# Kernel optimization log

Hardware: AMD Instinct MI355X
Metric: run time of the kernel (lower is better)

Reference implementation:

```python
import jax, jax.numpy as jnp
import numpy as np

LEFT = 16  # attention window size (previous `left` symbols incl. current)


def _make_history(symbols, left):
    """contexts[b, t, j] = symbols[b, t - (left-1-j)] for j in [0,left),
    padded with symbols[b, 0] for out-of-range positions (pad = symbols[:, :1])."""
    B, T = symbols.shape
    # (T, left) gather index matrix
    idx = jnp.arange(T)[:, None] - (left - 1 - jnp.arange(left))[None, :]
    valid = idx >= 0
    idx_c = jnp.clip(idx, 0, T - 1)
    ctx = symbols[:, idx_c]                                   # (B, T, left)
    pad = symbols[:, :1][:, :, None]                          # (B, 1, 1)
    return jnp.where(valid[None, :, :], ctx, pad)             # (B, T, left)


def setup_inputs() -> dict:
    key = jax.random.key(0)
    k1, k2, k3, k4 = jax.random.split(key, 4)
    B, T, V, D = 8, 2048, 256, 512
    symbols = jax.random.randint(k1, (B, T), 0, V, dtype=jnp.int32)
    encodings = jax.random.normal(k2, (B, T, D), dtype=jnp.float32)
    # keras 'uniform' initializer: U(-0.05, 0.05)
    M = jax.random.uniform(k3, (V, D), minval=-0.05, maxval=0.05, dtype=jnp.float32)
    C = jax.random.uniform(k4, (V, D), minval=-0.05, maxval=0.05, dtype=jnp.float32)
    return {"symbols": symbols, "encodings": encodings, "M": M, "C": C}


def reference(symbols, encodings, M, C):
    contexts = _make_history(symbols, LEFT)                   # (B, T, L) int
    Mg = M[contexts]                                          # (B, T, L, D)
    Cg = C[contexts]                                          # (B, T, L, D)
    scores = jnp.einsum('btld,btd->btl', Mg, encodings)       # (B, T, L)
    p = jax.nn.softmax(scores, axis=-1)                       # (B, T, L)
    compressed = jnp.einsum('btl,btld->btd', p, Cg)           # (B, T, D)
    output = jnp.concatenate([compressed, encodings], axis=-1)  # (B, T, 2D)
    return output, p
```

## Files before the change

### kernel.cpp

```cpp
#include <hip/hip_runtime.h>
#include <hip/hip_bf16.h>

#define B_ 8
#define T_ 2048
#define V_ 256
#define D_ 512
#define LEFT_ 16
#define C_LDW 520

typedef float f32x4 __attribute__((ext_vector_type(4)));
typedef short bf16x8 __attribute__((ext_vector_type(8)));
typedef unsigned long long u64;
union FragU { unsigned u[4]; u64 ull[2]; bf16x8 v; };

__device__ __forceinline__ unsigned pack_bf2(float a, float b) {
    __hip_bfloat162 h = __float22bfloat162_rn(make_float2(a, b));
    union { __hip_bfloat162 h; unsigned u; } c; c.h = h; return c.u;
}

#define SPART_OFF 33280
#define SMEM_BYTES (SPART_OFF + 8 * 16 * 36 * 4)

__global__ __launch_bounds__(512)
void attn_cell_kernel(const int* __restrict__ symbols,
                      const float* __restrict__ encodings,
                      const float* __restrict__ M,
                      const float* __restrict__ C,
                      float* __restrict__ out,
                      float* __restrict__ p_out) {
    __shared__ __align__(16) char smem[SMEM_BYTES];

    const int tid  = threadIdx.x;
    const int lane = tid & 63;
    const int w    = tid >> 6;
    const int q    = lane >> 4;
    const int t    = lane & 15;

    const int blk = blockIdx.x;
    const int b   = blk >> 7;
    const int t0  = (blk & 127) * 16;
    const int* symrow = symbols + b * T_;
    const size_t rowbase = (size_t)b * T_ + t0;

    {
        u64* r8 = (u64*)smem;
        #pragma unroll
        for (int i = tid; i < 2048; i += 512) {
            const int j = i >> 6;
            const int g = i & 63;
            int pos = t0 - (LEFT_ - 1) + j;
            pos = max(pos, 0); pos = min(pos, T_ - 1);
            const float* src = M + (size_t)symrow[pos] * D_ + g * 8;
            const float4 v0 = ((const float4*)src)[0];
            const float4 v1 = ((const float4*)src)[1];
            const u64 lo = (u64)pack_bf2(v0.x, v0.y) | ((u64)pack_bf2(v0.z, v0.w) << 32);
            const u64 hi = (u64)pack_bf2(v1.x, v1.y) | ((u64)pack_bf2(v1.z, v1.w) << 32);
            const int c = j & 7;
            r8[j * 128 + ((2 * g) ^ c)]     = lo;
            r8[j * 128 + ((2 * g + 1) ^ c)] = hi;
        }
    }
    __syncthreads();

    f32x4 acc0 = {0.f, 0.f, 0.f, 0.f}, acc1 = {0.f, 0.f, 0.f, 0.f};
    {
        const float* ebase = encodings + (rowbase + t) * D_;
        float* obase = out + (rowbase + t) * 1024 + D_;
        const u64* r8 = (const u64*)smem;
        const int c0 = t & 7;
        #pragma unroll
        for (int kc = 0; kc < 2; ++kc) {
            const int d0 = 64 * w + 32 * kc + 4 * q;
            const float4 e0 = *(const float4*)(ebase + d0);
            const float4 e1 = *(const float4*)(ebase + d0 + 16);
            *(float4*)(obase + d0)      = e0;
            *(float4*)(obase + d0 + 16) = e1;
            FragU bf;
            bf.u[0] = pack_bf2(e0.x, e0.y); bf.u[1] = pack_bf2(e0.z, e0.w);
            bf.u[2] = pack_bf2(e1.x, e1.y); bf.u[3] = pack_bf2(e1.z, e1.w);
            const int gb = 16 * w + 8 * kc + q;
            FragU a0, a1;
            a0.ull[0] = r8[t * 128        + ((gb)     ^ c0)];
            a0.ull[1] = r8[t * 128        + ((gb + 4) ^ c0)];
            a1.ull[0] = r8[(t + 16) * 128 + ((gb)     ^ c0)];
            a1.ull[1] = r8[(t + 16) * 128 + ((gb + 4) ^ c0)];
            acc0 = __builtin_amdgcn_mfma_f32_16x16x32_bf16(a0.v, bf.v, acc0, 0, 0, 0);
            acc1 = __builtin_amdgcn_mfma_f32_16x16x32_bf16(a1.v, bf.v, acc1, 0, 0, 0);
        }
    }
    {
        float* sp = (float*)(smem + SPART_OFF);
        *(f32x4*)&sp[(w * 16 + t) * 36 + 4 * q]      = acc0;
        *(f32x4*)&sp[(w * 16 + t) * 36 + 16 + 4 * q] = acc1;
    }
    __syncthreads();

    FragU pf;
    {
        const float* sp = (const float*)(smem + SPART_OFF);
        f32x4 s0 = *(const f32x4*)&sp[t * 36 + 4 * q];
        f32x4 s1 = *(const f32x4*)&sp[t * 36 + 16 + 4 * q];
        #pragma unroll
        for (int w2 = 1; w2 < 8; ++w2) {
            s0 += *(const f32x4*)&sp[(w2 * 16 + t) * 36 + 4 * q];
            s1 += *(const f32x4*)&sp[(w2 * 16 + t) * 36 + 16 + 4 * q];
        }
        float mx = -3.0e38f;
        #pragma unroll
        for (int r = 0; r < 4; ++r) {
            if ((unsigned)(4 * q + r - t) < 16u)      mx = fmaxf(mx, s0[r]);
            if ((unsigned)(4 * q + r + 16 - t) < 16u) mx = fmaxf(mx, s1[r]);
        }
        mx = fmaxf(mx, __shfl_xor(mx, 16));
        mx = fmaxf(mx, __shfl_xor(mx, 32));
        float p0[4], p1[4];
        float sum = 0.f;
        #pragma unroll
        for (int r = 0; r < 4; ++r) {
            const bool m0 = (unsigned)(4 * q + r - t) < 16u;
            const bool m1 = (unsigned)(4 * q + r + 16 - t) < 16u;
            p0[r] = m0 ? __expf(s0[r] - mx) : 0.f;
            p1[r] = m1 ? __expf(s1[r] - mx) : 0.f;
            sum += p0[r] + p1[r];
        }
        sum += __shfl_xor(sum, 16);
        sum += __shfl_xor(sum, 32);
        const float inv = 1.f / sum;
        #pragma unroll
        for (int r = 0; r < 4; ++r) { p0[r] *= inv; p1[r] *= inv; }

        if (w == 0) {
            #pragma unroll
            for (int r = 0; r < 4; ++r) {
                const int j0 = 4 * q + r;
                if ((unsigned)(j0 - t) < 16u)
                    p_out[(rowbase + t) * 16 + (j0 - t)] = p0[r];
                else
                    p_out[(rowbase + t) * 16 + (j0 + 16 - t)] = p1[r];
            }
        }
        pf.u[0] = pack_bf2(p0[0], p0[1]); pf.u[1] = pack_bf2(p0[2], p0[3]);
        pf.u[2] = pack_bf2(p1[0], p1[1]); pf.u[3] = pack_bf2(p1[2], p1[3]);
    }
    __syncthreads();

    {
        #pragma unroll
        for (int i = tid; i < 2048; i += 512) {
            const int j = i >> 6;
            const int g = i & 63;
            int pos = t0 - (LEFT_ - 1) + j;
            pos = max(pos, 0); pos = min(pos, T_ - 1);
            const float* src = C + (size_t)symrow[pos] * D_ + g * 8;
            const float4 v0 = ((const float4*)src)[0];
            const float4 v1 = ((const float4*)src)[1];
            u64* dst = (u64*)(smem + ((size_t)j * C_LDW + g * 8) * 2);
            dst[0] = (u64)pack_bf2(v0.x, v0.y) | ((u64)pack_bf2(v0.z, v0.w) << 32);
            dst[1] = (u64)pack_bf2(v1.x, v1.y) | ((u64)pack_bf2(v1.z, v1.w) << 32);
        }
    }
    __syncthreads();

    {
        const unsigned short* cb = (const unsigned short*)smem;
        #pragma unroll
        for (int m = 0; m < 4; ++m) {
            const int dc = w * 4 + m;
            const int dA = dc * 16 + t;
            unsigned short cbits[8];
            #pragma unroll
            for (int e = 0; e < 8; ++e) {
                const int j = 4 * q + (e & 3) + 16 * (e >> 2);
                cbits[e] = cb[j * C_LDW + dA];
            }
            FragU af;
            af.u[0] = cbits[0] | ((unsigned)cbits[1] << 16);
            af.u[1] = cbits[2] | ((unsigned)cbits[3] << 16);
            af.u[2] = cbits[4] | ((unsigned)cbits[5] << 16);
            af.u[3] = cbits[6] | ((unsigned)cbits[7] << 16);
            f32x4 o = {0.f, 0.f, 0.f, 0.f};
            o = __builtin_amdgcn_mfma_f32_16x16x32_bf16(af.v, pf.v, o, 0, 0, 0);
            float* ob = out + (rowbase + t) * 1024 + dc * 16 + 4 * q;
            *(float4*)ob = make_float4(o[0], o[1], o[2], o[3]);
        }
    }
}

extern "C" void kernel_launch(void* const* d_in, const int* in_sizes, int n_in,
                              void* d_out, int out_size, void* d_ws, size_t ws_size,
                              hipStream_t stream) {
    const int*   symbols   = (const int*)d_in[0];
    const float* encodings = (const float*)d_in[1];
    const float* M         = (const float*)d_in[2];
    const float* C         = (const float*)d_in[3];
    float* out   = (float*)d_out;
    float* p_out = out + (size_t)B_ * T_ * 1024;

    dim3 grid(B_ * (T_ / 16));
    attn_cell_kernel<<<grid, 512, 0, stream>>>(symbols, encodings, M, C, out, p_out);
}
```

Before: 32.88 us.

## Load M fragments directly from global and stage C early to drop barriers

```diff
diff --git a/kernel.cpp b/kernel.cpp
--- a/kernel.cpp
+++ b/kernel.cpp
@@ -18,9 +18,6 @@
     union { __hip_bfloat162 h; unsigned u; } c; c.h = h; return c.u;
 }
 
-#define SPART_OFF 33280
-#define SMEM_BYTES (SPART_OFF + 8 * 16 * 36 * 4)
-
 __global__ __launch_bounds__(512)
 void attn_cell_kernel(const int* __restrict__ symbols,
                       const float* __restrict__ encodings,
@@ -28,7 +25,8 @@
                       const float* __restrict__ C,
                       float* __restrict__ out,
                       float* __restrict__ p_out) {
-    __shared__ __align__(16) char smem[SMEM_BYTES];
+    __shared__ __align__(16) unsigned short cbuf[32 * C_LDW];
+    __shared__ __align__(16) float sp[8 * 16 * 36];
 
     const int tid  = threadIdx.x;
     const int lane = tid & 63;
@@ -42,32 +40,18 @@
     const int* symrow = symbols + b * T_;
     const size_t rowbase = (size_t)b * T_ + t0;
 
-    {
-        u64* r8 = (u64*)smem;
-        #pragma unroll
-        for (int i = tid; i < 2048; i += 512) {
-            const int j = i >> 6;
-            const int g = i & 63;
-            int pos = t0 - (LEFT_ - 1) + j;
-            pos = max(pos, 0); pos = min(pos, T_ - 1);
-            const float* src = M + (size_t)symrow[pos] * D_ + g * 8;
-            const float4 v0 = ((const float4*)src)[0];
-            const float4 v1 = ((const float4*)src)[1];
-            const u64 lo = (u64)pack_bf2(v0.x, v0.y) | ((u64)pack_bf2(v0.z, v0.w) << 32);
-            const u64 hi = (u64)pack_bf2(v1.x, v1.y) | ((u64)pack_bf2(v1.z, v1.w) << 32);
-            const int c = j & 7;
-            r8[j * 128 + ((2 * g) ^ c)]     = lo;
-            r8[j * 128 + ((2 * g + 1) ^ c)] = hi;
-        }
+    int sa[2];
+    #pragma unroll
+    for (int g = 0; g < 2; ++g) {
+        int pos = t0 + t + 16 * g - (LEFT_ - 1);
+        pos = max(pos, 0); pos = min(pos, T_ - 1);
+        sa[g] = symrow[pos];
     }
-    __syncthreads();
 
-    f32x4 acc0 = {0.f, 0.f, 0.f, 0.f}, acc1 = {0.f, 0.f, 0.f, 0.f};
+    FragU bf[2];
     {
         const float* ebase = encodings + (rowbase + t) * D_;
         float* obase = out + (rowbase + t) * 1024 + D_;
-        const u64* r8 = (const u64*)smem;
-        const int c0 = t & 7;
         #pragma unroll
         for (int kc = 0; kc < 2; ++kc) {
             const int d0 = 64 * w + 32 * kc + 4 * q;
@@ -75,29 +59,55 @@
             const float4 e1 = *(const float4*)(ebase + d0 + 16);
             *(float4*)(obase + d0)      = e0;
             *(float4*)(obase + d0 + 16) = e1;
-            FragU bf;
-            bf.u[0] = pack_bf2(e0.x, e0.y); bf.u[1] = pack_bf2(e0.z, e0.w);
-            bf.u[2] = pack_bf2(e1.x, e1.y); bf.u[3] = pack_bf2(e1.z, e1.w);
-            const int gb = 16 * w + 8 * kc + q;
-            FragU a0, a1;
-            a0.ull[0] = r8[t * 128        + ((gb)     ^ c0)];
-            a0.ull[1] = r8[t * 128        + ((gb + 4) ^ c0)];
-            a1.ull[0] = r8[(t + 16) * 128 + ((gb)     ^ c0)];
-            a1.ull[1] = r8[(t + 16) * 128 + ((gb + 4) ^ c0)];
-            acc0 = __builtin_amdgcn_mfma_f32_16x16x32_bf16(a0.v, bf.v, acc0, 0, 0, 0);
-            acc1 = __builtin_amdgcn_mfma_f32_16x16x32_bf16(a1.v, bf.v, acc1, 0, 0, 0);
+            bf[kc].u[0] = pack_bf2(e0.x, e0.y); bf[kc].u[1] = pack_bf2(e0.z, e0.w);
+            bf[kc].u[2] = pack_bf2(e1.x, e1.y); bf[kc].u[3] = pack_bf2(e1.z, e1.w);
         }
     }
-    {
-        float* sp = (float*)(smem + SPART_OFF);
-        *(f32x4*)&sp[(w * 16 + t) * 36 + 4 * q]      = acc0;
-        *(f32x4*)&sp[(w * 16 + t) * 36 + 16 + 4 * q] = acc1;
+
+    #pragma unroll
+    for (int i = tid; i < 2048; i += 512) {
+        const int j = i >> 6;
+        const int g = i & 63;
+        int pos = t0 - (LEFT_ - 1) + j;
+        pos = max(pos, 0); pos = min(pos, T_ - 1);
+        const float* src = C + (size_t)symrow[pos] * D_ + g * 8;
+        const float4 v0 = ((const float4*)src)[0];
+        const float4 v1 = ((const float4*)src)[1];
+        u64* dst = (u64*)&cbuf[j * C_LDW + g * 8];
+        dst[0] = (u64)pack_bf2(v0.x, v0.y) | ((u64)pack_bf2(v0.z, v0.w) << 32);
+        dst[1] = (u64)pack_bf2(v1.x, v1.y) | ((u64)pack_bf2(v1.z, v1.w) << 32);
     }
+
+    f32x4 acc0 = {0.f, 0.f, 0.f, 0.f}, acc1 = {0.f, 0.f, 0.f, 0.f};
+    #pragma unroll
+    for (int kc = 0; kc < 2; ++kc) {
+        const int k0 = 64 * w + 32 * kc + 4 * q;
+        {
+            const float* ma = M + (size_t)sa[0] * D_ + k0;
+            const float4 x0 = *(const float4*)ma;
+            const float4 x1 = *(const float4*)(ma + 16);
+            FragU af;
+            af.u[0] = pack_bf2(x0.x, x0.y); af.u[1] = pack_bf2(x0.z, x0.w);
+            af.u[2] = pack_bf2(x1.x, x1.y); af.u[3] = pack_bf2(x1.z, x1.w);
+            acc0 = __builtin_amdgcn_mfma_f32_16x16x32_bf16(af.v, bf[kc].v, acc0, 0, 0, 0);
+        }
+        {
+            const float* ma = M + (size_t)sa[1] * D_ + k0;
+            const float4 x0 = *(const float4*)ma;
+            const float4 x1 = *(const float4*)(ma + 16);
+            FragU af;
+            af.u[0] = pack_bf2(x0.x, x0.y); af.u[1] = pack_bf2(x0.z, x0.w);
+            af.u[2] = pack_bf2(x1.x, x1.y); af.u[3] = pack_bf2(x1.z, x1.w);
+            acc1 = __builtin_amdgcn_mfma_f32_16x16x32_bf16(af.v, bf[kc].v, acc1, 0, 0, 0);
+        }
+    }
+    *(f32x4*)&sp[(w * 16 + t) * 36 + 4 * q]      = acc0;
+    *(f32x4*)&sp[(w * 16 + t) * 36 + 16 + 4 * q] = acc1;
+
     __syncthreads();
 
     FragU pf;
     {
-        const float* sp = (const float*)(smem + SPART_OFF);
         f32x4 s0 = *(const f32x4*)&sp[t * 36 + 4 * q];
         f32x4 s1 = *(const f32x4*)&sp[t * 36 + 16 + 4 * q];
         #pragma unroll
@@ -142,27 +152,8 @@
         pf.u[0] = pack_bf2(p0[0], p0[1]); pf.u[1] = pack_bf2(p0[2], p0[3]);
         pf.u[2] = pack_bf2(p1[0], p1[1]); pf.u[3] = pack_bf2(p1[2], p1[3]);
     }
-    __syncthreads();
 
     {
-        #pragma unroll
-        for (int i = tid; i < 2048; i += 512) {
-            const int j = i >> 6;
-            const int g = i & 63;
-            int pos = t0 - (LEFT_ - 1) + j;
-            pos = max(pos, 0); pos = min(pos, T_ - 1);
-            const float* src = C + (size_t)symrow[pos] * D_ + g * 8;
-            const float4 v0 = ((const float4*)src)[0];
-            const float4 v1 = ((const float4*)src)[1];
-            u64* dst = (u64*)(smem + ((size_t)j * C_LDW + g * 8) * 2);
-            dst[0] = (u64)pack_bf2(v0.x, v0.y) | ((u64)pack_bf2(v0.z, v0.w) << 32);
-            dst[1] = (u64)pack_bf2(v1.x, v1.y) | ((u64)pack_bf2(v1.z, v1.w) << 32);
-        }
-    }
-    __syncthreads();
-
-    {
-        const unsigned short* cb = (const unsigned short*)smem;
         #pragma unroll
         for (int m = 0; m < 4; ++m) {
             const int dc = w * 4 + m;
@@ -171,7 +162,7 @@
             #pragma unroll
             for (int e = 0; e < 8; ++e) {
                 const int j = 4 * q + (e & 3) + 16 * (e >> 2);
-                cbits[e] = cb[j * C_LDW + dA];
+                cbits[e] = cbuf[j * C_LDW + dA];
             }
             FragU af;
             af.u[0] = cbits[0] | ((unsigned)cbits[1] << 16);
```

New measurement: 32.09 us. 1.02x faster.
